# Kernel tuning notes

Hardware: AMD Instinct MI355X
Metric: run time of the kernel (lower is better)

## Reference

```python
import jax, jax.numpy as jnp
import numpy as np

N = 50000      # nodes
E = 600000     # edges
G = 256        # graphs in batch
H = 128        # hidden channels
EPS = 1e-5     # batchnorm eps


def gcn_conv(x, W, b, src, dst, n):
    """PyG GCNConv: h = x W; symmetric-normalized aggregation with self-loops."""
    h = x @ W  # [n, H]
    ones = jnp.ones(src.shape[0], dtype=x.dtype)
    deg = jax.ops.segment_sum(ones, dst, num_segments=n) + 1.0  # in-degree + self-loop
    dis = jax.lax.rsqrt(deg)  # deg^{-1/2}
    msg = (dis[src] * dis[dst])[:, None] * h[src]  # [E, H] gathered messages
    agg = jax.ops.segment_sum(msg, dst, num_segments=n)
    return agg + (dis * dis)[:, None] * h + b  # self-loop contribution + bias


def batch_norm(x, gamma, beta):
    m = x.mean(axis=0)
    v = x.var(axis=0)  # biased variance, as torch BN uses for normalization
    return gamma * (x - m) * jax.lax.rsqrt(v + EPS) + beta


def setup_inputs() -> dict:
    key = jax.random.key(0)
    ks = jax.random.split(key, 12)
    x = jax.random.normal(ks[0], (N, H), dtype=jnp.float32)
    edge_index = jax.random.randint(ks[1], (2, E), 0, N, dtype=jnp.int32)
    batch = jnp.sort(jax.random.randint(ks[2], (N,), 0, G, dtype=jnp.int32))
    s = 1.0 / np.sqrt(H)
    W1 = jax.random.uniform(ks[3], (H, H), jnp.float32, -s, s)
    b1 = jnp.zeros((H,), jnp.float32)
    g1 = jnp.ones((H,), jnp.float32)
    be1 = jnp.zeros((H,), jnp.float32)
    W2 = jax.random.uniform(ks[4], (H, H), jnp.float32, -s, s)
    b2 = jnp.zeros((H,), jnp.float32)
    g2 = jnp.ones((H,), jnp.float32)
    be2 = jnp.zeros((H,), jnp.float32)
    W3 = jax.random.uniform(ks[5], (H, H), jnp.float32, -s, s)
    b3 = jnp.zeros((H,), jnp.float32)
    Wl = jax.random.uniform(ks[6], (H, 1), jnp.float32, -s, s)
    bl = jnp.zeros((1,), jnp.float32)
    return {"x": x, "edge_index": edge_index, "batch": batch,
            "W1": W1, "b1": b1, "g1": g1, "be1": be1,
            "W2": W2, "b2": b2, "g2": g2, "be2": be2,
            "W3": W3, "b3": b3, "Wl": Wl, "bl": bl}


def reference(x, edge_index, batch, W1, b1, g1, be1, W2, b2, g2, be2, W3, b3, Wl, bl):
    src, dst = edge_index[0], edge_index[1]
    h = gcn_conv(x, W1, b1, src, dst, N)
    h = jax.nn.relu(batch_norm(h, g1, be1))  # dropout is identity in eval mode
    h = gcn_conv(h, W2, b2, src, dst, N)
    h = jax.nn.relu(batch_norm(h, g2, be2))
    h = jax.nn.relu(gcn_conv(h, W3, b3, src, dst, N))
    sums = jax.ops.segment_sum(h, batch, num_segments=G)           # [G, H]
    cnt = jax.ops.segment_sum(jnp.ones((N,), h.dtype), batch, num_segments=G)
    pooled = sums / jnp.maximum(cnt, 1.0)[:, None]                  # global mean pool
    return pooled @ Wl + bl                                         # [G, 1]
```

## Files before the change

### kernel.cpp

```cpp
#include <hip/hip_runtime.h>
#include <cstdint>

#define NN 50000
#define NE 600000
#define NGR 256
#define HD 128
#define HD2 64
#define BN_EPS 1e-5f

static __device__ __forceinline__ unsigned f2bf(float f) {
  unsigned u = __float_as_uint(f);
  return (u + 0x7FFFu + ((u >> 16) & 1u)) >> 16;
}
static __device__ __forceinline__ float bf_lo(unsigned v) {
  return __uint_as_float(v << 16);
}
static __device__ __forceinline__ float bf_hi(unsigned v) {
  return __uint_as_float(v & 0xFFFF0000u);
}

__global__ void k_zero(float4* __restrict__ p, int n4) {
  int i = blockIdx.x * blockDim.x + threadIdx.x;
  if (i < n4) p[i] = make_float4(0.f, 0.f, 0.f, 0.f);
}

__global__ void k_count(const int* __restrict__ dst, int* __restrict__ cnt) {
  int i = blockIdx.x * blockDim.x + threadIdx.x;
  if (i < NE) atomicAdd(&cnt[dst[i]], 1);
}

__global__ __launch_bounds__(1024) void k_scan1(const int* __restrict__ cnt,
                                                int* __restrict__ rowptr,
                                                int* __restrict__ aux,
                                                float* __restrict__ dis) {
  __shared__ int sd[1024];
  int tid = threadIdx.x;
  int i = blockIdx.x * 1024 + tid;
  int v = (i < NN) ? cnt[i] : 0;
  if (i < NN) dis[i] = 1.0f / sqrtf((float)v + 1.0f);
  sd[tid] = v;
  __syncthreads();
  for (int off = 1; off < 1024; off <<= 1) {
    int t = (tid >= off) ? sd[tid - off] : 0;
    __syncthreads();
    sd[tid] += t;
    __syncthreads();
  }
  if (i < NN) rowptr[i + 1] = sd[tid];
  if (tid == 1023) aux[blockIdx.x] = sd[1023];
}

__global__ void k_scan2(const int* __restrict__ aux, int* __restrict__ auxsc, int nchunks) {
  if (threadIdx.x == 0 && blockIdx.x == 0) {
    int run = 0;
    for (int c = 0; c < nchunks; ++c) { auxsc[c] = run; run += aux[c]; }
  }
}

__global__ void k_scan3(int* __restrict__ rowptr, const int* __restrict__ auxsc) {
  int i = blockIdx.x * blockDim.x + threadIdx.x;
  if (i < NN) rowptr[i + 1] += auxsc[i >> 10];
  if (i == 0) rowptr[0] = 0;
}

__global__ void k_fill(const int* __restrict__ src, const int* __restrict__ dst,
                       const int* __restrict__ rowptr, int* __restrict__ fillp,
                       int* __restrict__ colidx) {
  int i = blockIdx.x * blockDim.x + threadIdx.x;
  if (i < NE) {
    int d = dst[i];
    int p = rowptr[d] + atomicAdd(&fillp[d], 1);
    colidx[p] = src[i];
  }
}

template<bool BN>
__global__ __launch_bounds__(256) void k_gemm(
    const float* __restrict__ X, const float* __restrict__ W,
    const float* __restrict__ scale, const float* __restrict__ shift,
    const float* __restrict__ dis, unsigned* __restrict__ HS) {
  __shared__ float xt[64][36];
  __shared__ float wt[32][132];
  int tid = threadIdx.x;
  int tc = tid & 15;
  int tr = tid >> 4;
  int row0 = blockIdx.x * 64;
  int r0 = tr * 4;
  float acc[4][8];
#pragma unroll
  for (int i = 0; i < 4; ++i)
#pragma unroll
    for (int j = 0; j < 8; ++j) acc[i][j] = 0.f;

  int lr = tid >> 2;
  int lk = (tid & 3) * 8;
  int wk = tid >> 3;
  int wc = (tid & 7) * 16;

  for (int kk = 0; kk < HD; kk += 32) {
    float4 a0 = make_float4(0.f, 0.f, 0.f, 0.f);
    float4 a1 = make_float4(0.f, 0.f, 0.f, 0.f);
    int row = row0 + lr;
    if (row < NN) {
      const float* xp = &X[(size_t)row * HD + kk + lk];
      a0 = *(const float4*)xp;
      a1 = *(const float4*)(xp + 4);
    }
    if constexpr (BN) {
      float4 sc0 = *(const float4*)&scale[kk + lk];
      float4 sc1 = *(const float4*)&scale[kk + lk + 4];
      float4 sh0 = *(const float4*)&shift[kk + lk];
      float4 sh1 = *(const float4*)&shift[kk + lk + 4];
      a0.x = fmaxf(fmaf(sc0.x, a0.x, sh0.x), 0.f);
      a0.y = fmaxf(fmaf(sc0.y, a0.y, sh0.y), 0.f);
      a0.z = fmaxf(fmaf(sc0.z, a0.z, sh0.z), 0.f);
      a0.w = fmaxf(fmaf(sc0.w, a0.w, sh0.w), 0.f);
      a1.x = fmaxf(fmaf(sc1.x, a1.x, sh1.x), 0.f);
      a1.y = fmaxf(fmaf(sc1.y, a1.y, sh1.y), 0.f);
      a1.z = fmaxf(fmaf(sc1.z, a1.z, sh1.z), 0.f);
      a1.w = fmaxf(fmaf(sc1.w, a1.w, sh1.w), 0.f);
    }
    *(float4*)&xt[lr][lk] = a0;
    *(float4*)&xt[lr][lk + 4] = a1;
    const float* wp = &W[(size_t)(kk + wk) * HD + wc];
    *(float4*)&wt[wk][wc]      = *(const float4*)(wp);
    *(float4*)&wt[wk][wc + 4]  = *(const float4*)(wp + 4);
    *(float4*)&wt[wk][wc + 8]  = *(const float4*)(wp + 8);
    *(float4*)&wt[wk][wc + 12] = *(const float4*)(wp + 12);
    __syncthreads();
#pragma unroll 4
    for (int k = 0; k < 32; ++k) {
      float av[4];
#pragma unroll
      for (int i = 0; i < 4; ++i) av[i] = xt[r0 + i][k];
      float2 bv[4];
#pragma unroll
      for (int j = 0; j < 4; ++j) bv[j] = *(const float2*)&wt[k][tc * 2 + 32 * j];
#pragma unroll
      for (int i = 0; i < 4; ++i)
#pragma unroll
        for (int j = 0; j < 4; ++j) {
          acc[i][2 * j]     = fmaf(av[i], bv[j].x, acc[i][2 * j]);
          acc[i][2 * j + 1] = fmaf(av[i], bv[j].y, acc[i][2 * j + 1]);
        }
    }
    __syncthreads();
  }
#pragma unroll
  for (int i = 0; i < 4; ++i) {
    int row = row0 + r0 + i;
    if (row < NN) {
      float dv = dis[row];
#pragma unroll
      for (int j = 0; j < 4; ++j) {
        unsigned p = (f2bf(acc[i][2 * j + 1] * dv) << 16) | f2bf(acc[i][2 * j] * dv);
        HS[(size_t)row * HD2 + tc + 16 * j] = p;
      }
    }
  }
}

template<int MODE>
__global__ __launch_bounds__(256) void k_agg(
    const unsigned* __restrict__ HS, const float* __restrict__ dis,
    const int* __restrict__ rowptr, const int* __restrict__ colidx,
    const float* __restrict__ bias,
    float* __restrict__ AGG, float* __restrict__ stats,
    const int* __restrict__ batch, const float* __restrict__ Wl,
    float* __restrict__ gsum, float* __restrict__ gcnt) {
  __shared__ float red[4][128];
  int tid = threadIdx.x;
  int lane = tid & 63;
  int wv = tid >> 6;
  int c0 = lane * 2;
  float b0 = bias[c0], b1 = bias[c0 + 1];
  float wl0 = 0.f, wl1 = 0.f;
  if (MODE == 1) { wl0 = Wl[c0]; wl1 = Wl[c0 + 1]; }
  float ssum0 = 0.f, ssum1 = 0.f, ssq0 = 0.f, ssq1 = 0.f;
  int stride = gridDim.x * 4;
  for (int i = blockIdx.x * 4 + wv; i < NN; i += stride) {
    unsigned sv = HS[(size_t)i * HD2 + lane];
    float ax = bf_lo(sv), ay = bf_hi(sv);
    float bx = 0.f, by = 0.f;
    float cx = 0.f, cy = 0.f;
    float dx = 0.f, dy = 0.f;
    int e0 = rowptr[i], e1 = rowptr[i + 1];
    int e = e0;
    for (; e + 7 < e1; e += 8) {
      int s0 = colidx[e];
      int s1 = colidx[e + 1];
      int s2 = colidx[e + 2];
      int s3 = colidx[e + 3];
      int s4 = colidx[e + 4];
      int s5 = colidx[e + 5];
      int s6 = colidx[e + 6];
      int s7 = colidx[e + 7];
      unsigned h0 = HS[(size_t)s0 * HD2 + lane];
      unsigned h1 = HS[(size_t)s1 * HD2 + lane];
      unsigned h2 = HS[(size_t)s2 * HD2 + lane];
      unsigned h3 = HS[(size_t)s3 * HD2 + lane];
      unsigned h4 = HS[(size_t)s4 * HD2 + lane];
      unsigned h5 = HS[(size_t)s5 * HD2 + lane];
      unsigned h6 = HS[(size_t)s6 * HD2 + lane];
      unsigned h7 = HS[(size_t)s7 * HD2 + lane];
      ax += bf_lo(h0); ay += bf_hi(h0);
      bx += bf_lo(h1); by += bf_hi(h1);
      cx += bf_lo(h2); cy += bf_hi(h2);
      dx += bf_lo(h3); dy += bf_hi(h3);
      ax += bf_lo(h4); ay += bf_hi(h4);
      bx += bf_lo(h5); by += bf_hi(h5);
      cx += bf_lo(h6); cy += bf_hi(h6);
      dx += bf_lo(h7); dy += bf_hi(h7);
    }
    for (; e + 3 < e1; e += 4) {
      int s0 = colidx[e];
      int s1 = colidx[e + 1];
      int s2 = colidx[e + 2];
      int s3 = colidx[e + 3];
      unsigned h0 = HS[(size_t)s0 * HD2 + lane];
      unsigned h1 = HS[(size_t)s1 * HD2 + lane];
      unsigned h2 = HS[(size_t)s2 * HD2 + lane];
      unsigned h3 = HS[(size_t)s3 * HD2 + lane];
      ax += bf_lo(h0); ay += bf_hi(h0);
      bx += bf_lo(h1); by += bf_hi(h1);
      cx += bf_lo(h2); cy += bf_hi(h2);
      dx += bf_lo(h3); dy += bf_hi(h3);
    }
    for (; e < e1; ++e) {
      int s0 = colidx[e];
      unsigned h0 = HS[(size_t)s0 * HD2 + lane];
      ax += bf_lo(h0); ay += bf_hi(h0);
    }
    float di = dis[i];
    float vx = fmaf(di, (ax + bx) + (cx + dx), b0);
    float vy = fmaf(di, (ay + by) + (cy + dy), b1);
    if (MODE == 0) {
      *(float2*)&AGG[(size_t)i * HD + c0] = make_float2(vx, vy);
      ssum0 += vx; ssum1 += vy;
      ssq0 = fmaf(vx, vx, ssq0);
      ssq1 = fmaf(vy, vy, ssq1);
    } else {
      vx = fmaxf(vx, 0.f);
      vy = fmaxf(vy, 0.f);
      float p = vx * wl0 + vy * wl1;
#pragma unroll
      for (int m = 32; m >= 1; m >>= 1) p += __shfl_xor(p, m);
      if (lane == 0) {
        int b = batch[i];
        atomicAdd(&gsum[b], p);
        atomicAdd(&gcnt[b], 1.0f);
      }
    }
  }
  if (MODE == 0) {
    red[wv][c0] = ssum0; red[wv][c0 + 1] = ssum1;
    __syncthreads();
    if (wv == 0) {
      float t0 = red[0][c0] + red[1][c0] + red[2][c0] + red[3][c0];
      float t1 = red[0][c0 + 1] + red[1][c0 + 1] + red[2][c0 + 1] + red[3][c0 + 1];
      atomicAdd(&stats[c0], t0);
      atomicAdd(&stats[c0 + 1], t1);
    }
    __syncthreads();
    red[wv][c0] = ssq0; red[wv][c0 + 1] = ssq1;
    __syncthreads();
    if (wv == 0) {
      float q0 = red[0][c0] + red[1][c0] + red[2][c0] + red[3][c0];
      float q1 = red[0][c0 + 1] + red[1][c0 + 1] + red[2][c0 + 1] + red[3][c0 + 1];
      atomicAdd(&stats[HD + c0], q0);
      atomicAdd(&stats[HD + c0 + 1], q1);
    }
  }
}

__global__ void k_bnfin(const float* __restrict__ stats, const float* __restrict__ gamma,
                        const float* __restrict__ beta, float* __restrict__ scale,
                        float* __restrict__ shift) {
  int c = threadIdx.x;
  float inv_n = 1.0f / (float)NN;
  float mean = stats[c] * inv_n;
  float var = stats[HD + c] * inv_n - mean * mean;
  float s = gamma[c] / sqrtf(var + BN_EPS);
  scale[c] = s;
  shift[c] = fmaf(-mean, s, beta[c]);
}

__global__ void k_final(const float* __restrict__ gsum, const float* __restrict__ gcnt,
                        const float* __restrict__ bl, float* __restrict__ out) {
  int g = threadIdx.x;
  out[g] = gsum[g] / fmaxf(gcnt[g], 1.0f) + bl[0];
}

extern "C" void kernel_launch(void* const* d_in, const int* in_sizes, int n_in,
                              void* d_out, int out_size, void* d_ws, size_t ws_size,
                              hipStream_t stream) {
  (void)in_sizes; (void)n_in; (void)out_size; (void)ws_size;
  const float* x   = (const float*)d_in[0];
  const int* ei    = (const int*)d_in[1];
  const int* batch = (const int*)d_in[2];
  const float* W1  = (const float*)d_in[3];
  const float* b1  = (const float*)d_in[4];
  const float* g1  = (const float*)d_in[5];
  const float* be1 = (const float*)d_in[6];
  const float* W2  = (const float*)d_in[7];
  const float* b2  = (const float*)d_in[8];
  const float* g2  = (const float*)d_in[9];
  const float* be2 = (const float*)d_in[10];
  const float* W3  = (const float*)d_in[11];
  const float* b3  = (const float*)d_in[12];
  const float* Wl  = (const float*)d_in[13];
  const float* bl  = (const float*)d_in[14];
  float* out = (float*)d_out;

  const int* srcv = ei;
  const int* dstv = ei + NE;

  unsigned* hs  = (unsigned*)d_ws;
  float* agg    = (float*)(hs + (size_t)NN * HD2);
  float* dis    = agg + (size_t)NN * HD;
  int*   rowptr = (int*)(dis + NN);
  int*   colidx = rowptr + (NN + 4);
  float* scale1 = (float*)(colidx + NE);
  float* shift1 = scale1 + HD;
  float* scale2 = shift1 + HD;
  float* shift2 = scale2 + HD;
  float* zbase  = shift2 + HD;
  int*   degc   = (int*)zbase;
  int*   fillp  = degc + NN;
  int*   aux    = fillp + NN;
  int*   auxsc  = aux + 64;
  float* stats1 = (float*)(auxsc + 64);
  float* stats2 = stats1 + 2 * HD;
  float* gsum   = stats2 + 2 * HD;
  float* gcnt   = gsum + NGR;
  float* zend   = gcnt + NGR;
  int n4 = (int)(((char*)zend - (char*)zbase) / 16);

  k_zero<<<(n4 + 255) / 256, 256, 0, stream>>>((float4*)zbase, n4);

  k_count<<<(NE + 255) / 256, 256, 0, stream>>>(dstv, degc);
  int nchunk = (NN + 1023) / 1024;
  k_scan1<<<nchunk, 1024, 0, stream>>>(degc, rowptr, aux, dis);
  k_scan2<<<1, 1, 0, stream>>>(aux, auxsc, nchunk);
  k_scan3<<<(NN + 255) / 256, 256, 0, stream>>>(rowptr, auxsc);
  k_fill<<<(NE + 255) / 256, 256, 0, stream>>>(srcv, dstv, rowptr, fillp, colidx);

  int gblk = (NN + 63) / 64;
  k_gemm<false><<<gblk, 256, 0, stream>>>(x, W1, nullptr, nullptr, dis, hs);
  k_agg<0><<<2048, 256, 0, stream>>>(hs, dis, rowptr, colidx, b1, agg, stats1,
                                     nullptr, nullptr, nullptr, nullptr);
  k_bnfin<<<1, HD, 0, stream>>>(stats1, g1, be1, scale1, shift1);
  k_gemm<true><<<gblk, 256, 0, stream>>>(agg, W2, scale1, shift1, dis, hs);
  k_agg<0><<<2048, 256, 0, stream>>>(hs, dis, rowptr, colidx, b2, agg, stats2,
                                     nullptr, nullptr, nullptr, nullptr);
  k_bnfin<<<1, HD, 0, stream>>>(stats2, g2, be2, scale2, shift2);
  k_gemm<true><<<gblk, 256, 0, stream>>>(agg, W3, scale2, shift2, dis, hs);
  k_agg<1><<<2048, 256, 0, stream>>>(hs, dis, rowptr, colidx, b3, nullptr, nullptr,
                                     batch, Wl, gsum, gcnt);
  k_final<<<1, NGR, 0, stream>>>(gsum, gcnt, bl, out);
}
```

Before: 729.6 us.

## Use bf16 MFMA for dense GEMM and store aggregation output in bf16

Replaces the FP32 SIMT tiled GEMM with a bf16 MFMA 16x16x32 kernel. Weights are pre-transposed and converted to bf16 by a small new kernel, and both operands are staged in XOR-swizzled LDS to avoid bank conflicts. The intermediate aggregation buffer is now stored as packed bf16 instead of fp32, halving its write and re-read traffic between layers. This trades some precision, since GEMM inputs and activations are rounded to bf16, for fewer bytes moved and matrix-core throughput. It also adds three extra small kernel launches.

```diff
diff --git a/kernel.cpp b/kernel.cpp
--- a/kernel.cpp
+++ b/kernel.cpp
@@ -7,6 +7,9 @@
 #define HD 128
 #define HD2 64
 #define BN_EPS 1e-5f
+
+typedef __attribute__((ext_vector_type(8))) short bf16x8;
+typedef __attribute__((ext_vector_type(4))) float f32x4;
 
 static __device__ __forceinline__ unsigned f2bf(float f) {
   unsigned u = __float_as_uint(f);
@@ -74,88 +77,94 @@
   }
 }
 
+__global__ void k_wt(const float* __restrict__ W, unsigned short* __restrict__ WT) {
+  int idx = blockIdx.x * 256 + threadIdx.x;
+  int k = idx >> 7, n = idx & 127;
+  WT[n * 128 + k] = (unsigned short)f2bf(W[idx]);
+}
+
 template<bool BN>
 __global__ __launch_bounds__(256) void k_gemm(
-    const float* __restrict__ X, const float* __restrict__ W,
+    const void* __restrict__ Xv, const unsigned short* __restrict__ WT,
     const float* __restrict__ scale, const float* __restrict__ shift,
     const float* __restrict__ dis, unsigned* __restrict__ HS) {
-  __shared__ float xt[64][36];
-  __shared__ float wt[32][132];
+  __shared__ unsigned short lw[128 * 128];
+  __shared__ unsigned short lx[64 * 128];
   int tid = threadIdx.x;
-  int tc = tid & 15;
-  int tr = tid >> 4;
   int row0 = blockIdx.x * 64;
-  int r0 = tr * 4;
-  float acc[4][8];
-#pragma unroll
-  for (int i = 0; i < 4; ++i)
-#pragma unroll
-    for (int j = 0; j < 8; ++j) acc[i][j] = 0.f;
-
-  int lr = tid >> 2;
-  int lk = (tid & 3) * 8;
-  int wk = tid >> 3;
-  int wc = (tid & 7) * 16;
-
-  for (int kk = 0; kk < HD; kk += 32) {
-    float4 a0 = make_float4(0.f, 0.f, 0.f, 0.f);
-    float4 a1 = make_float4(0.f, 0.f, 0.f, 0.f);
-    int row = row0 + lr;
+#pragma unroll
+  for (int i = 0; i < 8; ++i) {
+    int c2 = tid + 256 * i;
+    int n = c2 >> 4, c = c2 & 15;
+    uint4 v = *(const uint4*)&WT[n * 128 + c * 8];
+    *(uint4*)&lw[n * 128 + ((c ^ (n & 15)) << 3)] = v;
+  }
+#pragma unroll
+  for (int i = 0; i < 4; ++i) {
+    int c2 = tid + 256 * i;
+    int m = c2 >> 4, c = c2 & 15;
+    int row = row0 + m;
+    unsigned short h[8];
     if (row < NN) {
-      const float* xp = &X[(size_t)row * HD + kk + lk];
-      a0 = *(const float4*)xp;
-      a1 = *(const float4*)(xp + 4);
-    }
-    if constexpr (BN) {
-      float4 sc0 = *(const float4*)&scale[kk + lk];
-      float4 sc1 = *(const float4*)&scale[kk + lk + 4];
-      float4 sh0 = *(const float4*)&shift[kk + lk];
-      float4 sh1 = *(const float4*)&shift[kk + lk + 4];
-      a0.x = fmaxf(fmaf(sc0.x, a0.x, sh0.x), 0.f);
-      a0.y = fmaxf(fmaf(sc0.y, a0.y, sh0.y), 0.f);
-      a0.z = fmaxf(fmaf(sc0.z, a0.z, sh0.z), 0.f);
-      a0.w = fmaxf(fmaf(sc0.w, a0.w, sh0.w), 0.f);
-      a1.x = fmaxf(fmaf(sc1.x, a1.x, sh1.x), 0.f);
-      a1.y = fmaxf(fmaf(sc1.y, a1.y, sh1.y), 0.f);
-      a1.z = fmaxf(fmaf(sc1.z, a1.z, sh1.z), 0.f);
-      a1.w = fmaxf(fmaf(sc1.w, a1.w, sh1.w), 0.f);
-    }
-    *(float4*)&xt[lr][lk] = a0;
-    *(float4*)&xt[lr][lk + 4] = a1;
-    const float* wp = &W[(size_t)(kk + wk) * HD + wc];
-    *(float4*)&wt[wk][wc]      = *(const float4*)(wp);
-    *(float4*)&wt[wk][wc + 4]  = *(const float4*)(wp + 4);
-    *(float4*)&wt[wk][wc + 8]  = *(const float4*)(wp + 8);
-    *(float4*)&wt[wk][wc + 12] = *(const float4*)(wp + 12);
-    __syncthreads();
-#pragma unroll 4
-    for (int k = 0; k < 32; ++k) {
-      float av[4];
-#pragma unroll
-      for (int i = 0; i < 4; ++i) av[i] = xt[r0 + i][k];
-      float2 bv[4];
-#pragma unroll
-      for (int j = 0; j < 4; ++j) bv[j] = *(const float2*)&wt[k][tc * 2 + 32 * j];
-#pragma unroll
-      for (int i = 0; i < 4; ++i)
-#pragma unroll
-        for (int j = 0; j < 4; ++j) {
-          acc[i][2 * j]     = fmaf(av[i], bv[j].x, acc[i][2 * j]);
-          acc[i][2 * j + 1] = fmaf(av[i], bv[j].y, acc[i][2 * j + 1]);
-        }
-    }
-    __syncthreads();
-  }
-#pragma unroll
-  for (int i = 0; i < 4; ++i) {
-    int row = row0 + r0 + i;
-    if (row < NN) {
-      float dv = dis[row];
-#pragma unroll
-      for (int j = 0; j < 4; ++j) {
-        unsigned p = (f2bf(acc[i][2 * j + 1] * dv) << 16) | f2bf(acc[i][2 * j] * dv);
-        HS[(size_t)row * HD2 + tc + 16 * j] = p;
+      if constexpr (!BN) {
+        const float* X = (const float*)Xv;
+        const float* xp = &X[(size_t)row * HD + c * 8];
+        float4 a0 = *(const float4*)xp;
+        float4 a1 = *(const float4*)(xp + 4);
+        h[0] = (unsigned short)f2bf(a0.x); h[1] = (unsigned short)f2bf(a0.y);
+        h[2] = (unsigned short)f2bf(a0.z); h[3] = (unsigned short)f2bf(a0.w);
+        h[4] = (unsigned short)f2bf(a1.x); h[5] = (unsigned short)f2bf(a1.y);
+        h[6] = (unsigned short)f2bf(a1.z); h[7] = (unsigned short)f2bf(a1.w);
+      } else {
+        const unsigned* X = (const unsigned*)Xv;
+        uint4 pw = *(const uint4*)&X[(size_t)row * HD2 + c * 4];
+        float4 sc0 = *(const float4*)&scale[c * 8];
+        float4 sc1 = *(const float4*)&scale[c * 8 + 4];
+        float4 sh0 = *(const float4*)&shift[c * 8];
+        float4 sh1 = *(const float4*)&shift[c * 8 + 4];
+        h[0] = (unsigned short)f2bf(fmaxf(fmaf(sc0.x, bf_lo(pw.x), sh0.x), 0.f));
+        h[1] = (unsigned short)f2bf(fmaxf(fmaf(sc0.y, bf_hi(pw.x), sh0.y), 0.f));
+        h[2] = (unsigned short)f2bf(fmaxf(fmaf(sc0.z, bf_lo(pw.y), sh0.z), 0.f));
+        h[3] = (unsigned short)f2bf(fmaxf(fmaf(sc0.w, bf_hi(pw.y), sh0.w), 0.f));
+        h[4] = (unsigned short)f2bf(fmaxf(fmaf(sc1.x, bf_lo(pw.z), sh1.x), 0.f));
+        h[5] = (unsigned short)f2bf(fmaxf(fmaf(sc1.y, bf_hi(pw.z), sh1.y), 0.f));
+        h[6] = (unsigned short)f2bf(fmaxf(fmaf(sc1.z, bf_lo(pw.w), sh1.z), 0.f));
+        h[7] = (unsigned short)f2bf(fmaxf(fmaf(sc1.w, bf_hi(pw.w), sh1.w), 0.f));
       }
+    } else {
+#pragma unroll
+      for (int j = 0; j < 8; ++j) h[j] = 0;
+    }
+    *(uint4*)&lx[m * 128 + ((c ^ (m & 15)) << 3)] = *(uint4*)h;
+  }
+  __syncthreads();
+
+  int l = tid & 63, w = tid >> 6;
+  int cl = l & 15, g = l >> 4;
+  f32x4 acc[8];
+#pragma unroll
+  for (int nb = 0; nb < 8; ++nb)
+#pragma unroll
+    for (int z = 0; z < 4; ++z) acc[nb][z] = 0.f;
+
+#pragma unroll
+  for (int ks = 0; ks < 4; ++ks) {
+    int chunk = ((ks * 4 + g) ^ cl) << 3;
+    bf16x8 b = *(bf16x8*)&lx[(w * 16 + cl) * 128 + chunk];
+#pragma unroll
+    for (int nb = 0; nb < 8; ++nb) {
+      bf16x8 a = *(bf16x8*)&lw[(nb * 16 + cl) * 128 + chunk];
+      acc[nb] = __builtin_amdgcn_mfma_f32_16x16x32_bf16(a, b, acc[nb], 0, 0, 0);
+    }
+  }
+  int m = row0 + w * 16 + cl;
+  if (m < NN) {
+    float dv = dis[m];
+#pragma unroll
+    for (int nb = 0; nb < 8; ++nb) {
+      unsigned w0 = (f2bf(acc[nb][1] * dv) << 16) | f2bf(acc[nb][0] * dv);
+      unsigned w1 = (f2bf(acc[nb][3] * dv) << 16) | f2bf(acc[nb][2] * dv);
+      *(uint2*)&HS[(size_t)m * HD2 + nb * 8 + g * 2] = make_uint2(w0, w1);
     }
   }
 }
@@ -165,7 +174,7 @@
     const unsigned* __restrict__ HS, const float* __restrict__ dis,
     const int* __restrict__ rowptr, const int* __restrict__ colidx,
     const float* __restrict__ bias,
-    float* __restrict__ AGG, float* __restrict__ stats,
+    unsigned* __restrict__ AGG, float* __restrict__ stats,
     const int* __restrict__ batch, const float* __restrict__ Wl,
     float* __restrict__ gsum, float* __restrict__ gcnt) {
   __shared__ float red[4][128];
@@ -235,7 +244,7 @@
     float vx = fmaf(di, (ax + bx) + (cx + dx), b0);
     float vy = fmaf(di, (ay + by) + (cy + dy), b1);
     if (MODE == 0) {
-      *(float2*)&AGG[(size_t)i * HD + c0] = make_float2(vx, vy);
+      AGG[(size_t)i * HD2 + lane] = (f2bf(vy) << 16) | f2bf(vx);
       ssum0 += vx; ssum1 += vy;
       ssq0 = fmaf(vx, vx, ssq0);
       ssq1 = fmaf(vy, vy, ssq1);
@@ -315,25 +324,26 @@
   const int* srcv = ei;
   const int* dstv = ei + NE;
 
-  unsigned* hs  = (unsigned*)d_ws;
-  float* agg    = (float*)(hs + (size_t)NN * HD2);
-  float* dis    = agg + (size_t)NN * HD;
-  int*   rowptr = (int*)(dis + NN);
-  int*   colidx = rowptr + (NN + 4);
-  float* scale1 = (float*)(colidx + NE);
-  float* shift1 = scale1 + HD;
-  float* scale2 = shift1 + HD;
-  float* shift2 = scale2 + HD;
-  float* zbase  = shift2 + HD;
-  int*   degc   = (int*)zbase;
-  int*   fillp  = degc + NN;
-  int*   aux    = fillp + NN;
-  int*   auxsc  = aux + 64;
-  float* stats1 = (float*)(auxsc + 64);
-  float* stats2 = stats1 + 2 * HD;
-  float* gsum   = stats2 + 2 * HD;
-  float* gcnt   = gsum + NGR;
-  float* zend   = gcnt + NGR;
+  unsigned* hs   = (unsigned*)d_ws;
+  unsigned* aggb = hs + (size_t)NN * HD2;
+  float* dis     = (float*)(aggb + (size_t)NN * HD2);
+  int*   rowptr  = (int*)(dis + NN);
+  int*   colidx  = rowptr + (NN + 4);
+  unsigned short* wtb = (unsigned short*)(colidx + NE);
+  float* scale1  = (float*)(wtb + 128 * 128);
+  float* shift1  = scale1 + HD;
+  float* scale2  = shift1 + HD;
+  float* shift2  = scale2 + HD;
+  float* zbase   = shift2 + HD;
+  int*   degc    = (int*)zbase;
+  int*   fillp   = degc + NN;
+  int*   aux     = fillp + NN;
+  int*   auxsc   = aux + 64;
+  float* stats1  = (float*)(auxsc + 64);
+  float* stats2  = stats1 + 2 * HD;
+  float* gsum    = stats2 + 2 * HD;
+  float* gcnt    = gsum + NGR;
+  float* zend    = gcnt + NGR;
   int n4 = (int)(((char*)zend - (char*)zbase) / 16);
 
   k_zero<<<(n4 + 255) / 256, 256, 0, stream>>>((float4*)zbase, n4);
@@ -346,15 +356,18 @@
   k_fill<<<(NE + 255) / 256, 256, 0, stream>>>(srcv, dstv, rowptr, fillp, colidx);
 
   int gblk = (NN + 63) / 64;
-  k_gemm<false><<<gblk, 256, 0, stream>>>(x, W1, nullptr, nullptr, dis, hs);
-  k_agg<0><<<2048, 256, 0, stream>>>(hs, dis, rowptr, colidx, b1, agg, stats1,
+  k_wt<<<64, 256, 0, stream>>>(W1, wtb);
+  k_gemm<false><<<gblk, 256, 0, stream>>>(x, wtb, nullptr, nullptr, dis, hs);
+  k_agg<0><<<2048, 256, 0, stream>>>(hs, dis, rowptr, colidx, b1, aggb, stats1,
                                      nullptr, nullptr, nullptr, nullptr);
   k_bnfin<<<1, HD, 0, stream>>>(stats1, g1, be1, scale1, shift1);
-  k_gemm<true><<<gblk, 256, 0, stream>>>(agg, W2, scale1, shift1, dis, hs);
-  k_agg<0><<<2048, 256, 0, stream>>>(hs, dis, rowptr, colidx, b2, agg, stats2,
+  k_wt<<<64, 256, 0, stream>>>(W2, wtb);
+  k_gemm<true><<<gblk, 256, 0, stream>>>(aggb, wtb, scale1, shift1, dis, hs);
+  k_agg<0><<<2048, 256, 0, stream>>>(hs, dis, rowptr, colidx, b2, aggb, stats2,
                                      nullptr, nullptr, nullptr, nullptr);
   k_bnfin<<<1, HD, 0, stream>>>(stats2, g2, be2, scale2, shift2);
-  k_gemm<true><<<gblk, 256, 0, stream>>>(agg, W3, scale2, shift2, dis, hs);
+  k_wt<<<64, 256, 0, stream>>>(W3, wtb);
+  k_gemm<true><<<gblk, 256, 0, stream>>>(aggb, wtb, scale2, shift2, dis, hs);
   k_agg<1><<<2048, 256, 0, stream>>>(hs, dis, rowptr, colidx, b3, nullptr, nullptr,
                                      batch, Wl, gsum, gcnt);
   k_final<<<1, NGR, 0, stream>>>(gsum, gcnt, bl, out);
```

After: 698.4 us. 4.3% less time.
